# Optimization experiments

Measured on AMD Instinct MI355X. Metric: run time of the kernel, lower is better.

## Reference

```python
import jax, jax.numpy as jnp
import numpy as np

N = 8192      # nodes
K_NN = 32     # kNN neighbors (module default k=32)
E = N * 16    # edges for TAGConv graph
EPS = 1e-5    # BatchNorm eps


def setup_inputs() -> dict:
    key = jax.random.key(0)
    ks = iter(jax.random.split(key, 64))
    def lin(i, o):
        return jax.random.normal(next(ks), (i, o), jnp.float32) / np.float32(np.sqrt(i))
    def vec(c, scale=0.02):
        return jax.random.normal(next(ks), (c,), jnp.float32) * scale
    inp = {}
    inp["pos"] = jax.random.normal(next(ks), (N, 3), jnp.float32)
    inp["x"] = jax.random.normal(next(ks), (N, 4), jnp.float32)
    inp["edge_index"] = jax.random.randint(next(ks), (2, E), 0, N, jnp.int32)
    # conv1 edge-MLP [2*3, 64, 64, 64]
    inp["mlp1_W1"] = lin(6, 64)
    inp["mlp1_W23"] = jnp.stack([lin(64, 64), lin(64, 64)])
    inp["mlp1_b"] = jnp.stack([vec(64) for _ in range(3)])
    inp["mlp1_g"] = 1.0 + jnp.stack([vec(64) for _ in range(3)])
    inp["mlp1_beta"] = jnp.stack([vec(64) for _ in range(3)])
    # conv2 edge-MLP [2*64, 128]
    inp["mlp2_W"] = lin(128, 128); inp["mlp2_b"] = vec(128)
    inp["mlp2_g"] = 1.0 + vec(128); inp["mlp2_beta"] = vec(128)
    # lin1 MLP [128+64, 512]
    inp["lin1_W"] = lin(192, 512); inp["lin1_b"] = vec(512)
    inp["lin1_g"] = 1.0 + vec(512); inp["lin1_beta"] = vec(512)
    # TAGConv(4,64,K=3) and TAGConv(64,128,K=3): K+1 hop weights each, shared bias
    inp["tag1_W"] = jnp.stack([lin(4, 64) for _ in range(4)]); inp["tag1_b"] = vec(64)
    inp["tag2_W"] = jnp.stack([lin(64, 128) for _ in range(4)]); inp["tag2_b"] = vec(128)
    # lin_gcnn1 MLP [128+64, 512]
    inp["lin2_W"] = lin(192, 512); inp["lin2_b"] = vec(512)
    inp["lin2_g"] = 1.0 + vec(512); inp["lin2_beta"] = vec(512)
    # mix_output: MLP[1024,512] -> Dropout -> MLP[512,256] -> Dropout -> Lin(256,1)
    inp["mix1_W"] = lin(1024, 512); inp["mix1_b"] = vec(512)
    inp["mix1_g"] = 1.0 + vec(512); inp["mix1_beta"] = vec(512)
    inp["mix2_W"] = lin(512, 256); inp["mix2_b"] = vec(256)
    inp["mix2_g"] = 1.0 + vec(256); inp["mix2_beta"] = vec(256)
    inp["out_W"] = lin(256, 1); inp["out_b"] = vec(1)
    return inp


def _bn_relu_lin(h, W, b, g, beta):
    # Seq(Linear, ReLU, BatchNorm1d) with training-mode (batch) statistics
    h = jax.nn.relu(h @ W + b)
    mu = jnp.mean(h, axis=0)
    var = jnp.var(h, axis=0)
    return g * (h - mu) * jax.lax.rsqrt(var + EPS) + beta


def _knn_idx(x, k):
    # brute-force kNN (loop=False: self excluded); indices are non-differentiable
    x = jax.lax.stop_gradient(x)
    sq = jnp.sum(x * x, axis=1)
    d = sq[:, None] + sq[None, :] - 2.0 * (x @ x.T)   # [N,N] squared dists
    n = x.shape[0]
    d = d.at[jnp.arange(n), jnp.arange(n)].set(jnp.inf)
    _, idx = jax.lax.top_k(-d, k)
    return idx                                        # [N,k]


def _edge_conv(x, k, mlp_fn):
    # DynamicEdgeConv: kNN graph on x, message MLP([x_i, x_j - x_i]), max-aggregate
    idx = _knn_idx(x, k)
    xj = x[idx]                                       # [N,k,C]
    xi = jnp.broadcast_to(x[:, None, :], xj.shape)
    e = jnp.concatenate([xi, xj - xi], axis=-1).reshape(-1, 2 * x.shape[1])
    h = mlp_fn(e)                                     # [N*k, C_out]
    return jnp.max(h.reshape(x.shape[0], k, -1), axis=1)


def _tag_conv(x, W, b, row, col, norm):
    # TAGConv: out = sum_{m=0..K} (D^-1/2 A D^-1/2)^m x @ W_m + b
    out = x @ W[0]
    h = x
    for m in range(1, W.shape[0]):
        h = jax.ops.segment_sum(norm[:, None] * h[row], col, num_segments=x.shape[0])
        out = out + h @ W[m]
    return out + b


def reference(pos, x, edge_index, mlp1_W1, mlp1_W23, mlp1_b, mlp1_g, mlp1_beta,
              mlp2_W, mlp2_b, mlp2_g, mlp2_beta, lin1_W, lin1_b, lin1_g, lin1_beta,
              tag1_W, tag1_b, tag2_W, tag2_b, lin2_W, lin2_b, lin2_g, lin2_beta,
              mix1_W, mix1_b, mix1_g, mix1_beta, mix2_W, mix2_b, mix2_g, mix2_beta,
              out_W, out_b):
    def mlp1(e):
        h = _bn_relu_lin(e, mlp1_W1, mlp1_b[0], mlp1_g[0], mlp1_beta[0])
        h = _bn_relu_lin(h, mlp1_W23[0], mlp1_b[1], mlp1_g[1], mlp1_beta[1])
        return _bn_relu_lin(h, mlp1_W23[1], mlp1_b[2], mlp1_g[2], mlp1_beta[2])
    def mlp2(e):
        return _bn_relu_lin(e, mlp2_W, mlp2_b, mlp2_g, mlp2_beta)

    # --- DGCNN branch on positions ---
    x1 = _edge_conv(pos, K_NN, mlp1)                  # [N,64]
    x2 = _edge_conv(x1, K_NN, mlp2)                   # [N,128]
    out_dg = _bn_relu_lin(jnp.concatenate([x1, x2], axis=1),
                          lin1_W, lin1_b, lin1_g, lin1_beta)  # [N,512]

    # --- TAGConv branch on node features ---
    row, col = edge_index[0], edge_index[1]
    deg = jax.ops.segment_sum(jnp.ones(row.shape[0], x.dtype), col, num_segments=x.shape[0])
    dinv = jnp.where(deg > 0, jax.lax.rsqrt(jnp.maximum(deg, 1.0)), 0.0)
    norm = dinv[row] * dinv[col]
    g1 = jax.nn.relu(_tag_conv(x, tag1_W, tag1_b, row, col, norm))    # [N,64]
    g2 = jax.nn.relu(_tag_conv(g1, tag2_W, tag2_b, row, col, norm))   # [N,128]
    out_g = _bn_relu_lin(jnp.concatenate([g1, g2], axis=1),
                         lin2_W, lin2_b, lin2_g, lin2_beta)           # [N,512]

    # --- mix head (dropout = identity in eval) ---
    h = jnp.concatenate([out_dg, out_g], axis=1)      # [N,1024]
    h = _bn_relu_lin(h, mix1_W, mix1_b, mix1_g, mix1_beta)
    h = _bn_relu_lin(h, mix2_W, mix2_b, mix2_g, mix2_beta)
    return h @ out_W + out_b                          # [N,1]
```

## Files before the change

### kernel.cpp

```cpp
#include <hip/hip_runtime.h>
#include <cstdint>
#include <cstddef>

#define BN_EPS 1e-5f
#define K1CAP 1024
#define K2CAP 640

typedef short short8 __attribute__((ext_vector_type(8)));
typedef float f32x4 __attribute__((ext_vector_type(4)));
typedef unsigned long long ull;

__device__ __forceinline__ unsigned int ordf(float d) {
  unsigned int u = __float_as_uint(d);
  return (u >> 31) ? ~u : (u | 0x80000000u);
}
__device__ __forceinline__ unsigned short f2bf(float f) {
  unsigned u = __float_as_uint(f);
  u += 0x7fffu + ((u >> 16) & 1u);
  return (unsigned short)(u >> 16);
}
__device__ __forceinline__ float bf2f(unsigned short h) {
  return __uint_as_float(((unsigned)h) << 16);
}

#define BPAD 72

__global__ __launch_bounds__(256)
void mk_gemm_mfma(const float* __restrict__ A,
                  const short* __restrict__ A8h, const short* __restrict__ A8l,
                  const float* __restrict__ src, const int* __restrict__ gidx, int srcC,
                  const float* __restrict__ bnA,
                  const short* __restrict__ Wh, const short* __restrict__ Wl,
                  int ldk, int koff, int lda,
                  const float* __restrict__ bias,
                  float* __restrict__ C, short* __restrict__ Ch, short* __restrict__ Cl,
                  int ldc,
                  int M, int N, int K, int flags,
                  float* __restrict__ statsP,
                  float* __restrict__ mxp, float* __restrict__ mnp) {
  __shared__ short Ah[64][BPAD], Al[64][BPAD], Bh[64][BPAD], Bl[64][BPAD];
  __shared__ float ssum[64], ssq[64];
  int tid = threadIdx.x, lane = tid & 63, wid = tid >> 6;
  int wr = wid >> 1, wc = wid & 1;
  int r0 = blockIdx.x * 64, n0 = blockIdx.y * 64;
  int sr = tid >> 2, sc = (tid & 3) * 16;
  f32x4 zero4 = {0.f, 0.f, 0.f, 0.f};
  f32x4 acc[2][2] = {{zero4, zero4}, {zero4, zero4}};
  short8 rAh[2], rAl[2], rBh[2], rBl[2];

  auto stage = [&](int kt) {
    const short* bh = &Wh[(size_t)(n0 + sr) * ldk + koff + kt + sc];
    const short* bl = &Wl[(size_t)(n0 + sr) * ldk + koff + kt + sc];
    rBh[0] = *(const short8*)bh; rBh[1] = *(const short8*)(bh + 8);
    rBl[0] = *(const short8*)bl; rBl[1] = *(const short8*)(bl + 8);
    if (A8h) {
      const short* ah = &A8h[(size_t)(r0 + sr) * lda + kt + sc];
      const short* al = &A8l[(size_t)(r0 + sr) * lda + kt + sc];
      rAh[0] = *(const short8*)ah; rAh[1] = *(const short8*)(ah + 8);
      rAl[0] = *(const short8*)al; rAl[1] = *(const short8*)(al + 8);
    } else {
      float v[16];
      if (flags & 32) {
        int gr = r0 + sr;
        int i = gr >> 5; int j = gidx[gr];
        const float* pi = &A[(size_t)i * srcC + kt + sc];
        const float* pj = &src[(size_t)j * srcC + kt + sc];
        float va[16], vb[16];
        *(float4*)&va[0]  = *(const float4*)&pi[0];
        *(float4*)&va[4]  = *(const float4*)&pi[4];
        *(float4*)&va[8]  = *(const float4*)&pi[8];
        *(float4*)&va[12] = *(const float4*)&pi[12];
        *(float4*)&vb[0]  = *(const float4*)&pj[0];
        *(float4*)&vb[4]  = *(const float4*)&pj[4];
        *(float4*)&vb[8]  = *(const float4*)&pj[8];
        *(float4*)&vb[12] = *(const float4*)&pj[12];
#pragma unroll
        for (int e = 0; e < 16; ++e) v[e] = fmaxf(va[e] + vb[e], 0.f);
      } else {
        const float* ap = &A[(size_t)(r0 + sr) * lda + kt + sc];
        *(float4*)&v[0]  = *(const float4*)&ap[0];
        *(float4*)&v[4]  = *(const float4*)&ap[4];
        *(float4*)&v[8]  = *(const float4*)&ap[8];
        *(float4*)&v[12] = *(const float4*)&ap[12];
      }
      if (bnA) {
#pragma unroll
        for (int e = 0; e < 16; ++e) {
          int gk = kt + sc + e;
          v[e] = fmaf(bnA[gk], v[e], bnA[1024 + gk]);
        }
      }
#pragma unroll
      for (int e = 0; e < 16; ++e) {
        unsigned short h = f2bf(v[e]);
        rAh[e >> 3][e & 7] = (short)h;
        rAl[e >> 3][e & 7] = (short)f2bf(v[e] - bf2f(h));
      }
    }
  };

  stage(0);
  for (int kt = 0; kt < K; kt += 64) {
    *(short8*)&Ah[sr][sc]     = rAh[0];
    *(short8*)&Ah[sr][sc + 8] = rAh[1];
    *(short8*)&Al[sr][sc]     = rAl[0];
    *(short8*)&Al[sr][sc + 8] = rAl[1];
    *(short8*)&Bh[sr][sc]     = rBh[0];
    *(short8*)&Bh[sr][sc + 8] = rBh[1];
    *(short8*)&Bl[sr][sc]     = rBl[0];
    *(short8*)&Bl[sr][sc + 8] = rBl[1];
    __syncthreads();
    if (kt + 64 < K) stage(kt + 64);
    int ar = wr * 32 + (lane & 15);
    int br = wc * 32 + (lane & 15);
#pragma unroll
    for (int kk = 0; kk < 2; ++kk) {
      int kof = kk * 32 + (lane >> 4) * 8;
      short8 a_h[2], a_l[2], b_h[2], b_l[2];
#pragma unroll
      for (int t = 0; t < 2; ++t) {
        a_h[t] = *(const short8*)&Ah[ar + t * 16][kof];
        a_l[t] = *(const short8*)&Al[ar + t * 16][kof];
        b_h[t] = *(const short8*)&Bh[br + t * 16][kof];
        b_l[t] = *(const short8*)&Bl[br + t * 16][kof];
      }
#pragma unroll
      for (int mt = 0; mt < 2; ++mt)
#pragma unroll
        for (int nt = 0; nt < 2; ++nt) {
          acc[mt][nt] = __builtin_amdgcn_mfma_f32_16x16x32_bf16(a_h[mt], b_h[nt], acc[mt][nt], 0, 0, 0);
          acc[mt][nt] = __builtin_amdgcn_mfma_f32_16x16x32_bf16(a_h[mt], b_l[nt], acc[mt][nt], 0, 0, 0);
          acc[mt][nt] = __builtin_amdgcn_mfma_f32_16x16x32_bf16(a_l[mt], b_h[nt], acc[mt][nt], 0, 0, 0);
        }
    }
    __syncthreads();
  }
  bool dostat = (flags & 8) != 0, domx = (flags & 16) != 0;
  float lsum[2] = {0.f, 0.f}, lsq[2] = {0.f, 0.f};
  float lmx[2] = {-3.4e38f, -3.4e38f}, lmn[2] = {3.4e38f, 3.4e38f};
#pragma unroll
  for (int nt = 0; nt < 2; ++nt) {
    int gc = n0 + wc * 32 + nt * 16 + (lane & 15);
#pragma unroll
    for (int mt = 0; mt < 2; ++mt)
#pragma unroll
      for (int i = 0; i < 4; ++i) {
        int gr = r0 + wr * 32 + mt * 16 + (lane >> 4) * 4 + i;
        float v = acc[mt][nt][i];
        if (bias) v += bias[gc];
        if (flags & 1) v += C[(size_t)gr * ldc + gc];
        if (flags & 2) v = fmaxf(v, 0.f);
        if (!domx) {
          if (flags & 128) {
            int gj = srcC + gc;
            unsigned kk2 = (gr == gj) ? 0xFFFFFFFFu
                                      : ordf(src[gr] + src[gj] - 2.f * v);
            ((unsigned*)C)[(size_t)gr * ldc + gc] = kk2;
          } else if (flags & 64) {
            unsigned short hh = f2bf(v);
            Ch[(size_t)gr * ldc + gc] = (short)hh;
            Cl[(size_t)gr * ldc + gc] = (short)f2bf(v - bf2f(hh));
          } else {
            C[(size_t)gr * ldc + gc] = v;
          }
        }
        lsum[nt] += v; lsq[nt] = fmaf(v, v, lsq[nt]);
        lmx[nt] = fmaxf(lmx[nt], v); lmn[nt] = fminf(lmn[nt], v);
      }
  }
  if (dostat || domx) {
#pragma unroll
    for (int nt = 0; nt < 2; ++nt) {
#pragma unroll
      for (int m = 16; m <= 32; m <<= 1) {
        lsum[nt] += __shfl_xor(lsum[nt], m, 64);
        lsq[nt] += __shfl_xor(lsq[nt], m, 64);
        lmx[nt] = fmaxf(lmx[nt], __shfl_xor(lmx[nt], m, 64));
        lmn[nt] = fminf(lmn[nt], __shfl_xor(lmn[nt], m, 64));
      }
    }
    if (domx && lane < 16) {
      int node = blockIdx.x * 2 + wr;
#pragma unroll
      for (int nt = 0; nt < 2; ++nt) {
        int gc = n0 + wc * 32 + nt * 16 + lane;
        mxp[(size_t)node * N + gc] = lmx[nt];
        mnp[(size_t)node * N + gc] = lmn[nt];
      }
    }
    if (dostat) {
      if (tid < 64) { ssum[tid] = 0.f; ssq[tid] = 0.f; }
      __syncthreads();
      if (lane < 16) {
#pragma unroll
        for (int nt = 0; nt < 2; ++nt) {
          int ct = wc * 32 + nt * 16 + lane;
          atomicAdd(&ssum[ct], lsum[nt]);
          atomicAdd(&ssq[ct], lsq[nt]);
        }
      }
      __syncthreads();
      if (tid < 64) {
        int slot = blockIdx.x & 63;
        int gc = n0 + tid;
        atomicAdd(&statsP[(size_t)slot * 1024 + gc], ssum[tid]);
        atomicAdd(&statsP[(size_t)slot * 1024 + 512 + gc], ssq[tid]);
      }
    }
  }
}

__global__ void mk_wcvt(const float* __restrict__ W, short* __restrict__ Wh,
                        short* __restrict__ Wl, int K, int N) {
  int g = blockIdx.x * 256 + threadIdx.x;
  if (g >= K * N) return;
  int k = g / N, n = g - k * N;
  float v = W[g];
  unsigned short h = f2bf(v);
  Wh[(size_t)n * K + k] = (short)h;
  Wl[(size_t)n * K + k] = (short)f2bf(v - bf2f(h));
}
__global__ void mk_wcvts(const float* __restrict__ W, const float* __restrict__ a,
                         short* __restrict__ Wh, short* __restrict__ Wl, int K, int N) {
  int g = blockIdx.x * 256 + threadIdx.x;
  if (g >= K * N) return;
  int k = g / N, n = g - k * N;
  float v = a[k] * W[g];
  unsigned short h = f2bf(v);
  Wh[(size_t)n * K + k] = (short)h;
  Wl[(size_t)n * K + k] = (short)f2bf(v - bf2f(h));
}
__global__ void mk_biasfold(const float* __restrict__ W, const float* __restrict__ bv,
                            const float* __restrict__ b0, float* __restrict__ bo,
                            int K, int N) {
  int col = blockIdx.x * 4 + (threadIdx.x >> 6);
  int lane = threadIdx.x & 63;
  if (col >= N) return;
  float s = 0.f;
  for (int k = lane; k < K; k += 64) s = fmaf(bv[k], W[(size_t)k * N + col], s);
#pragma unroll
  for (int off = 32; off; off >>= 1) s += __shfl_xor(s, off, 64);
  if (lane == 0) bo[col] = b0[col] + s;
}
__global__ void mk_wcvt2(const float* __restrict__ W, short* __restrict__ Dh,
                         short* __restrict__ Dl, short* __restrict__ Vh,
                         short* __restrict__ Vl) {
  int g = blockIdx.x * 256 + threadIdx.x;
  if (g >= 64 * 128) return;
  int k = g >> 7, n = g & 127;
  float u = W[k * 128 + n], vv = W[(64 + k) * 128 + n];
  float d = u - vv;
  unsigned short h = f2bf(d);
  Dh[n * 64 + k] = (short)h; Dl[n * 64 + k] = (short)f2bf(d - bf2f(h));
  h = f2bf(vv);
  Vh[n * 64 + k] = (short)h; Vl[n * 64 + k] = (short)f2bf(vv - bf2f(h));
}

__global__ void mk_conv1nodes(const float* __restrict__ pos, const float* __restrict__ W1,
                              const float* __restrict__ b1, float* __restrict__ Pp,
                              float* __restrict__ Qn) {
  int g = blockIdx.x * 256 + threadIdx.x;
  if (g >= 8192 * 64) return;
  int i = g >> 6, c = g & 63;
  float p0 = pos[i * 3], p1 = pos[i * 3 + 1], p2 = pos[i * 3 + 2];
  float q = p0 * W1[192 + c] + p1 * W1[256 + c] + p2 * W1[320 + c];
  Qn[g] = q;
  Pp[g] = p0 * W1[c] + p1 * W1[64 + c] + p2 * W1[128 + c] - q + b1[c];
}

__global__ __launch_bounds__(256)
void mk_stats1(const float* __restrict__ Pp, const float* __restrict__ Qn,
               const int* __restrict__ idx1, float* __restrict__ statsP) {
  __shared__ int sidx[512];
  int tid = threadIdx.x;
  int c = tid & 63, grp = tid >> 6;
  int nb = blockIdx.x * 16;
  if (tid < 256) {
    sidx[tid] = idx1[nb * 32 + tid];
    sidx[tid + 256] = idx1[nb * 32 + 256 + tid];
  }
  __syncthreads();
  float s = 0.f, q = 0.f;
  for (int ln = 0; ln < 16; ++ln) {
    float pv = Pp[(size_t)(nb + ln) * 64 + c];
    for (int e = grp; e < 32; e += 4) {
      int j = sidx[ln * 32 + e];
      float v = fmaxf(pv + Qn[(size_t)j * 64 + c], 0.f);
      s += v; q = fmaf(v, v, q);
    }
  }
  int slot = (blockIdx.x * 4 + grp) & 63;
  atomicAdd(&statsP[(size_t)slot * 1024 + c], s);
  atomicAdd(&statsP[(size_t)slot * 1024 + 512 + c], q);
}

__global__ __launch_bounds__(128)
void mk_econv2(const float* __restrict__ R, const float* __restrict__ T,
               const int* __restrict__ st_i, float* __restrict__ mxp,
               float* __restrict__ mnp, float* __restrict__ statsP) {
  __shared__ int sidx[256];
  int tid = threadIdx.x;
  int nb = blockIdx.x * 8;
  sidx[tid] = st_i[nb * 32 + tid];
  sidx[tid + 128] = st_i[nb * 32 + 128 + tid];
  __syncthreads();
  float s = 0.f, q = 0.f;
  for (int ln = 0; ln < 8; ++ln) {
    int i = nb + ln;
    float rv = R[(size_t)i * 128 + tid];
    float mx = -3.4e38f, mn = 3.4e38f;
    for (int e = 0; e < 32; ++e) {
      int j = sidx[ln * 32 + e];
      float v = fmaxf(rv + T[(size_t)j * 128 + tid], 0.f);
      mx = fmaxf(mx, v); mn = fminf(mn, v);
      s += v; q = fmaf(v, v, q);
    }
    mxp[(size_t)i * 128 + tid] = mx;
    mnp[(size_t)i * 128 + tid] = mn;
  }
  int slot = blockIdx.x & 63;
  atomicAdd(&statsP[(size_t)slot * 1024 + tid], s);
  atomicAdd(&statsP[(size_t)slot * 1024 + 512 + tid], q);
}

__global__ void mk_bnfinS(const float* __restrict__ sb, const float* __restrict__ g,
                          const float* __restrict__ beta, float* __restrict__ bno,
                          float Minv, int Cdim) {
  int c = blockIdx.x * 256 + threadIdx.x;
  if (c >= Cdim) return;
  float s = 0.f, q = 0.f;
  for (int sl = 0; sl < 64; ++sl) {
    s += sb[(size_t)sl * 1024 + c];
    q += sb[(size_t)sl * 1024 + 512 + c];
  }
  float mu = s * Minv;
  float var = q * Minv - mu * mu;
  float a = g[c] * rsqrtf(var + BN_EPS);
  bno[c] = a;
  bno[1024 + c] = beta[c] - a * mu;
}

__global__ void mk_finx1(const float* __restrict__ mx, const float* __restrict__ mn,
                         const float* __restrict__ bn, float* __restrict__ xc,
                         short* __restrict__ x1h, short* __restrict__ x1l) {
  int g = blockIdx.x * 256 + threadIdx.x;
  if (g >= 8192 * 64) return;
  int i = g >> 6, c = g & 63;
  float a = bn[c], b = bn[1024 + c];
  float v = (a > 0.f) ? fmaf(a, mx[g], b) : fmaf(a, mn[g], b);
  xc[(size_t)i * 192 + c] = v;
  unsigned short h = f2bf(v);
  x1h[g] = (short)h;
  x1l[g] = (short)f2bf(v - bf2f(h));
}
__global__ void mk_finx2(const float* __restrict__ mx, const float* __restrict__ mn,
                         const float* __restrict__ bn, float* __restrict__ xcB) {
  int g = blockIdx.x * 256 + threadIdx.x;
  if (g >= 8192 * 128) return;
  int i = g >> 7, c = g & 127;
  float a = bn[c], b = bn[1024 + c];
  xcB[(size_t)i * 192 + c] = (a > 0.f) ? fmaf(a, mx[g], b) : fmaf(a, mn[g], b);
}

__global__ void mk_posq(const float* __restrict__ pos, float4* __restrict__ posq) {
  int i = blockIdx.x * 256 + threadIdx.x;
  if (i >= 8192) return;
  float x = pos[i * 3], y = pos[i * 3 + 1], z = pos[i * 3 + 2];
  float s = fmaf(z, z, fmaf(y, y, x * x));
  posq[i] = make_float4(x, y, z, s);
}

__device__ __forceinline__ unsigned wave_kth8(unsigned v) {
  unsigned T = 0;
#pragma unroll
  for (int b = 31; b >= 0; --b) {
    unsigned cand = T | (1u << b);
    int c = __popcll(__ballot(v < cand));
    if (c < 8) T = cand;
  }
  return T;
}

__global__ __launch_bounds__(256)
void mk_knn1(const float4* __restrict__ posq, int* __restrict__ idxout) {
  __shared__ ull buf[K1CAP];
  __shared__ unsigned Tw[4];
  __shared__ unsigned cnt;
  int q = blockIdx.x, tid = threadIdx.x;
  int lane = tid & 63, wid = tid >> 6;
  float4 pq = posq[q];
  if (tid == 0) cnt = 0;
  unsigned key[32];
  unsigned vmin = 0xFFFFFFFFu;
#pragma unroll
  for (int c = 0; c < 32; ++c) {
    int j = c * 256 + tid;
    float4 pj = posq[j];
    float d = pq.w + pj.w - 2.f * (pq.x * pj.x + pq.y * pj.y + pq.z * pj.z);
    unsigned k = (j == q) ? 0xFFFFFFFFu : ordf(d);
    key[c] = k;
    vmin = vmin < k ? vmin : k;
  }
  unsigned T = wave_kth8(vmin);
  if (lane == 0) Tw[wid] = T;
  __syncthreads();
  unsigned Tmax = max(max(Tw[0], Tw[1]), max(Tw[2], Tw[3]));
#pragma unroll
  for (int c = 0; c < 32; ++c) {
    if (key[c] <= Tmax) {
      int j = c * 256 + tid;
      unsigned s = atomicAdd(&cnt, 1u);
      if (s < K1CAP) buf[s] = (((ull)key[c]) << 32) | (unsigned)j;
    }
  }
  __syncthreads();
  int m = cnt < (unsigned)K1CAP ? (int)cnt : K1CAP;
  for (int e = tid; e < m; e += 256) {
    ull mine = buf[e];
    int rank = 0;
    for (int f = 0; f < m; ++f) rank += (buf[f] < mine) ? 1 : 0;
    if (rank < 32) idxout[q * 32 + rank] = (int)(unsigned)(mine & 0xFFFFFFFFu);
  }
}

__global__ __launch_bounds__(256)
void mk_knn2(const unsigned* __restrict__ Kb, int c0, int first,
             unsigned* __restrict__ st_k, int* __restrict__ st_i) {
  __shared__ ull buf[K2CAP];
  __shared__ unsigned Tw[4];
  __shared__ unsigned cnt;
  int q = blockIdx.x, tid = threadIdx.x;
  int lane = tid & 63, wid = tid >> 6;
  if (tid == 0) cnt = 0;
  unsigned key[16];
  unsigned vmin = 0xFFFFFFFFu;
#pragma unroll
  for (int c = 0; c < 16; ++c) {
    unsigned k = Kb[(size_t)q * 4096 + c * 256 + tid];
    key[c] = k;
    vmin = vmin < k ? vmin : k;
  }
  unsigned T = wave_kth8(vmin);
  if (lane == 0) Tw[wid] = T;
  __syncthreads();
  unsigned Tmax = max(max(Tw[0], Tw[1]), max(Tw[2], Tw[3]));
#pragma unroll
  for (int c = 0; c < 16; ++c) {
    if (key[c] <= Tmax) {
      int j = c0 + c * 256 + tid;
      unsigned s = atomicAdd(&cnt, 1u);
      if (s < K2CAP) buf[s] = (((ull)key[c]) << 32) | (unsigned)j;
    }
  }
  if (!first && tid < 32) {
    ull k = (((ull)st_k[q * 32 + tid]) << 32) | (unsigned)st_i[q * 32 + tid];
    unsigned s = atomicAdd(&cnt, 1u);
    if (s < K2CAP) buf[s] = k;
  }
  __syncthreads();
  int m = cnt < (unsigned)K2CAP ? (int)cnt : K2CAP;
  for (int e = tid; e < m; e += 256) {
    ull mine = buf[e];
    int rank = 0;
    for (int f = 0; f < m; ++f) rank += (buf[f] < mine) ? 1 : 0;
    if (rank < 32) {
      st_k[q * 32 + rank] = (unsigned)(mine >> 32);
      st_i[q * 32 + rank] = (int)(unsigned)(mine & 0xFFFFFFFFu);
    }
  }
}

#define GBM 64
#define GBN 64
#define GBK 16

__global__ __launch_bounds__(256)
void mk_gemm(const float* __restrict__ A, const float* __restrict__ W, int ldw,
             const float* __restrict__ bias, float* __restrict__ C, int ldc,
             int M, int N, int K, int flags) {
  __shared__ float As[GBK][GBM + 4];
  __shared__ float Ws[GBK][GBN];
  int tid = threadIdx.x;
  int r0 = blockIdx.x * GBM, n0 = blockIdx.y * GBN;
  int ty = tid >> 4, tx = tid & 15;
  float acc[4][4] = {};
  for (int kt = 0; kt < K; kt += GBK) {
#pragma unroll
    for (int it = 0; it < 4; ++it) {
      int l = it * 256 + tid;
      int r = l >> 4, kk = l & 15;
      int gr = r0 + r, gk = kt + kk;
      float v = 0.f;
      if (gk < K && gr < M) v = A[(size_t)gr * K + gk];
      As[kk][r] = v;
      int kw = l >> 6, nw = l & 63;
      int gkw = kt + kw;
      Ws[kw][nw] = (gkw < K && (n0 + nw) < N) ? W[(size_t)gkw * ldw + n0 + nw] : 0.f;
    }
    __syncthreads();
#pragma unroll
    for (int kk = 0; kk < GBK; ++kk) {
      float4 a4 = *(const float4*)&As[kk][ty * 4];
      float4 b4 = *(const float4*)&Ws[kk][tx * 4];
      float av[4] = {a4.x, a4.y, a4.z, a4.w};
      float bv[4] = {b4.x, b4.y, b4.z, b4.w};
#pragma unroll
      for (int i = 0; i < 4; ++i)
#pragma unroll
        for (int j = 0; j < 4; ++j)
          acc[i][j] = fmaf(av[i], bv[j], acc[i][j]);
    }
    __syncthreads();
  }
#pragma unroll
  for (int i = 0; i < 4; ++i) {
    int gr = r0 + ty * 4 + i;
    if (gr >= M) continue;
#pragma unroll
    for (int j = 0; j < 4; ++j) {
      int gc = n0 + tx * 4 + j;
      if (gc >= N) continue;
      float v = acc[i][j];
      if (bias) v += bias[gc];
      if (flags & 1) v += C[(size_t)gr * ldc + gc];
      if (flags & 2) v = fmaxf(v, 0.f);
      C[(size_t)gr * ldc + gc] = v;
    }
  }
}

__global__ void mk_sqnorm(const float* __restrict__ x, int ld, float* __restrict__ sq,
                          int Npts, int Cdim) {
  int i = blockIdx.x * blockDim.x + threadIdx.x;
  if (i >= Npts) return;
  float s = 0.f;
  for (int c = 0; c < Cdim; ++c) { float v = x[(size_t)i * ld + c]; s = fmaf(v, v, s); }
  sq[i] = s;
}

__global__ void mk_count(const int* __restrict__ col, int* __restrict__ cnt, int E) {
  int e = blockIdx.x * 256 + threadIdx.x;
  if (e < E) atomicAdd(&cnt[col[e]], 1);
}
__global__ __launch_bounds__(1024)
void mk_scan(const int* __restrict__ cnt, int* __restrict__ offp,
             int* __restrict__ cur, float* __restrict__ dinvf) {
  __shared__ int wsum[16];
  __shared__ int wexc[16];
  int t = threadIdx.x, lane = t & 63, w = t >> 6;
  int v[8]; int s = 0;
  int base = t * 8;
#pragma unroll
  for (int k = 0; k < 8; ++k) { v[k] = s; s += cnt[base + k]; }
  int sc = s;
#pragma unroll
  for (int off2 = 1; off2 < 64; off2 <<= 1) {
    int n = __shfl_up(sc, off2, 64);
    if (lane >= off2) sc += n;
  }
  if (lane == 63) wsum[w] = sc;
  __syncthreads();
  if (w == 0) {
    int x = (lane < 16) ? wsum[lane] : 0;
    int scx = x;
#pragma unroll
    for (int off2 = 1; off2 < 16; off2 <<= 1) {
      int n = __shfl_up(scx, off2, 64);
      if (lane >= off2) scx += n;
    }
    if (lane < 16) wexc[lane] = scx - x;
  }
  __syncthreads();
  int texc = wexc[w] + (sc - s);
#pragma unroll
  for (int k = 0; k < 8; ++k) {
    int o = texc + v[k];
    offp[base + k] = o;
    cur[base + k] = o;
    int d = cnt[base + k];
    dinvf[base + k] = (d > 0) ? rsqrtf((float)(d < 1 ? 1 : d)) : 0.f;
  }
  if (t == 1023) offp[8192] = texc + s;
}
__global__ void mk_fill(const int* __restrict__ row, const int* __restrict__ col,
                        const float* __restrict__ dinvf, int* __restrict__ cur,
                        int* __restrict__ crow, float* __restrict__ cw, int E) {
  int e = blockIdx.x * 256 + threadIdx.x;
  if (e >= E) return;
  int c = col[e], r = row[e];
  int s = atomicAdd(&cur[c], 1);
  crow[s] = r;
  cw[s] = dinvf[r] * dinvf[c];
}
__global__ void mk_prop64(const float* __restrict__ in, int in_ld,
                          const int* __restrict__ offp, const int* __restrict__ crow,
                          const float* __restrict__ cw, float* __restrict__ out, int out_ld) {
  int gid = blockIdx.x * 256 + threadIdx.x;
  if (gid >= 8192 * 16) return;
  int col = gid >> 4, c4 = (gid & 15) * 4;
  int s0 = offp[col], s1 = offp[col + 1];
  float a0 = 0, a1 = 0, a2 = 0, a3 = 0;
  for (int s = s0; s < s1; ++s) {
    int r = crow[s]; float w = cw[s];
    float4 v = *(const float4*)&in[(size_t)r * in_ld + c4];
    a0 = fmaf(w, v.x, a0); a1 = fmaf(w, v.y, a1);
    a2 = fmaf(w, v.z, a2); a3 = fmaf(w, v.w, a3);
  }
  float4 o = {a0, a1, a2, a3};
  *(float4*)&out[(size_t)col * out_ld + c4] = o;
}
__global__ void mk_prop4(const float* __restrict__ in, int in_ld,
                         const int* __restrict__ offp, const int* __restrict__ crow,
                         const float* __restrict__ cw, float* __restrict__ out, int out_ld) {
  int col = blockIdx.x * 256 + threadIdx.x;
  if (col >= 8192) return;
  int s0 = offp[col], s1 = offp[col + 1];
  float a0 = 0, a1 = 0, a2 = 0, a3 = 0;
  for (int s = s0; s < s1; ++s) {
    int r = crow[s]; float w = cw[s];
    float4 v = *(const float4*)&in[(size_t)r * in_ld];
    a0 = fmaf(w, v.x, a0); a1 = fmaf(w, v.y, a1);
    a2 = fmaf(w, v.z, a2); a3 = fmaf(w, v.w, a3);
  }
  float4 o = {a0, a1, a2, a3};
  *(float4*)&out[(size_t)col * out_ld] = o;
}
__global__ void mk_pack4(const float* __restrict__ xin, float* __restrict__ H1) {
  int g = blockIdx.x * 256 + threadIdx.x;
  if (g >= 8192 * 4) return;
  H1[(size_t)(g >> 2) * 16 + (g & 3)] = xin[g];
}
__global__ void mk_copy64(const float* __restrict__ gcv, float* __restrict__ H2) {
  int g = blockIdx.x * 256 + threadIdx.x;
  if (g >= 8192 * 64) return;
  H2[(size_t)(g >> 6) * 256 + (g & 63)] = gcv[(size_t)(g >> 6) * 192 + (g & 63)];
}

__global__ __launch_bounds__(256)
void mk_gemv_out(const float* __restrict__ h, const float* __restrict__ bn,
                 const float* __restrict__ w, const float* __restrict__ b,
                 float* __restrict__ out, int Npts) {
  int row = blockIdx.x * 4 + (threadIdx.x >> 6);
  int lane = threadIdx.x & 63;
  if (row >= Npts) return;
  int c = lane * 4;
  float4 v = *(const float4*)&h[(size_t)row * 256 + c];
  float s = (bn[c] * v.x + bn[1024 + c]) * w[c]
          + (bn[c + 1] * v.y + bn[1024 + c + 1]) * w[c + 1]
          + (bn[c + 2] * v.z + bn[1024 + c + 2]) * w[c + 2]
          + (bn[c + 3] * v.w + bn[1024 + c + 3]) * w[c + 3];
#pragma unroll
  for (int off = 32; off; off >>= 1) s += __shfl_xor(s, off, 64);
  if (lane == 0) out[row] = s + b[0];
}

extern "C" void kernel_launch(void* const* d_in, const int* in_sizes, int n_in,
                              void* d_out, int out_size, void* d_ws, size_t ws_size,
                              hipStream_t stream) {
  const int N = 8192;
  const int NE = N * 32;
  const float* pos = (const float*)d_in[0];
  const float* xin = (const float*)d_in[1];
  const int* ei = (const int*)d_in[2];
  const int E = in_sizes[2] / 2;
  const int* erow = ei;
  const int* ecol = ei + E;
  const float* mlp1_W1  = (const float*)d_in[3];
  const float* mlp1_W23 = (const float*)d_in[4];
  const float* mlp1_b   = (const float*)d_in[5];
  const float* mlp1_g   = (const float*)d_in[6];
  const float* mlp1_be  = (const float*)d_in[7];
  const float* mlp2_W   = (const float*)d_in[8];
  const float* mlp2_b   = (const float*)d_in[9];
  const float* mlp2_g   = (const float*)d_in[10];
  const float* mlp2_be  = (const float*)d_in[11];
  const float* lin1_W   = (const float*)d_in[12];
  const float* lin1_b   = (const float*)d_in[13];
  const float* lin1_g   = (const float*)d_in[14];
  const float* lin1_be  = (const float*)d_in[15];
  const float* tag1_W   = (const float*)d_in[16];
  const float* tag1_b   = (const float*)d_in[17];
  const float* tag2_W   = (const float*)d_in[18];
  const float* tag2_b   = (const float*)d_in[19];
  const float* lin2_W   = (const float*)d_in[20];
  const float* lin2_b   = (const float*)d_in[21];
  const float* lin2_g   = (const float*)d_in[22];
  const float* lin2_be  = (const float*)d_in[23];
  const float* mix1_W   = (const float*)d_in[24];
  const float* mix1_b   = (const float*)d_in[25];
  const float* mix1_g   = (const float*)d_in[26];
  const float* mix1_be  = (const float*)d_in[27];
  const float* mix2_W   = (const float*)d_in[28];
  const float* mix2_b   = (const float*)d_in[29];
  const float* mix2_g   = (const float*)d_in[30];
  const float* mix2_be  = (const float*)d_in[31];
  const float* outW     = (const float*)d_in[32];
  const float* outB     = (const float*)d_in[33];

  char* base = (char*)d_ws;
  size_t off = 0;
  auto alloc = [&](size_t b) -> void* {
    void* p = base + off;
    off += (b + 255) & ~(size_t)255;
    return p;
  };
  float* BIG = (float*)alloc(134217728ull);
  short* h2_h  = (short*)BIG;
  short* h2_l  = (short*)((char*)BIG + 33554432);
  unsigned* Kb = (unsigned*)BIG;
  short* mhcat_h = (short*)BIG;
  short* mhcat_l = (short*)((char*)BIG + 16777216);
  short* mh1_h   = (short*)((char*)BIG + 33554432);
  short* mh1_l   = (short*)((char*)BIG + 41943040);
  float* mh2     = (float*)((char*)BIG + 50331648);
  float* H2      = BIG + 16777216;
  int*   idx1 = (int*)alloc((size_t)NE * 4);
  unsigned* st_k = (unsigned*)alloc((size_t)NE * 4);
  int*   st_i = (int*)alloc((size_t)NE * 4);
  float* xc  = (float*)alloc((size_t)N * 192 * 4);
  float* gc  = (float*)alloc((size_t)N * 192 * 4);
  float4* posq = (float4*)alloc((size_t)N * 16);
  float* sqx = (float*)alloc((size_t)N * 4);
  float* Pp  = (float*)alloc((size_t)N * 64 * 4);
  float* Qn  = (float*)alloc((size_t)N * 64 * 4);
  float* Rb  = (float*)alloc((size_t)N * 128 * 4);
  float* Tb  = (float*)alloc((size_t)N * 128 * 4);
  float* mx1 = (float*)alloc((size_t)N * 64 * 4);
  float* mn1 = (float*)alloc((size_t)N * 64 * 4);
  float* mx2 = (float*)alloc((size_t)N * 128 * 4);
  float* mn2 = (float*)alloc((size_t)N * 128 * 4);
  float* H1  = (float*)alloc((size_t)N * 16 * 4);
  float* dinvf = (float*)alloc((size_t)N * 4);
  int* cnt     = (int*)alloc((size_t)N * 4);
  int* csr_off = (int*)alloc((size_t)(N + 1) * 4);
  int* cursor  = (int*)alloc((size_t)N * 4);
  int* csr_row = (int*)alloc((size_t)E * 4);
  float* csr_w = (float*)alloc((size_t)E * 4);
  float* slotAll = (float*)alloc((size_t)8 * 64 * 1024 * 4);
  auto slot = [&](int i) { return slotAll + (size_t)i * 64 * 1024; };
  float* bnb = (float*)alloc(8 * 2048 * 4);
  auto bnp = [&](int i) { return bnb + (size_t)i * 2048; };
  float* bnM = bnp(4);
  float* bias1f = (float*)alloc(512 * 4);
  float* bias2f = (float*)alloc(256 * 4);
  float* biasA  = (float*)alloc(64 * 4);
  float* biasB  = (float*)alloc(64 * 4);
  auto salloc = [&](size_t n) { return (short*)alloc(n * 2); };
  short* w23a_h = salloc(4096);   short* w23a_l = salloc(4096);
  short* w23b_h = salloc(4096);   short* w23b_l = salloc(4096);
  short* wd2_h  = salloc(8192);   short* wd2_l  = salloc(8192);
  short* wv2_h  = salloc(8192);   short* wv2_l  = salloc(8192);
  short* wl1_h  = salloc(98304);  short* wl1_l  = salloc(98304);
  short* wt2_h  = salloc(32768);  short* wt2_l  = salloc(32768);
  short* wl2_h  = salloc(98304);  short* wl2_l  = salloc(98304);
  short* wx1_h  = salloc(524288); short* wx1_l  = salloc(524288);
  short* wx2_h  = salloc(131072); short* wx2_l  = salloc(131072);
  short* x1h    = salloc(524288); short* x1l    = salloc(524288);

  auto gemmF = [&](const float* A, const short* A8h, const short* A8l,
                   const float* src, const int* gidx, int srcC, const float* bnA,
                   const short* Wh_, const short* Wl_, int ldk, int koff, int lda,
                   const float* bias, float* Cp, short* Chp, short* Clp, int ldc,
                   int M, int Nn, int Kk, int flags,
                   float* stP = nullptr, float* mxP = nullptr, float* mnP = nullptr) {
    dim3 g(M / 64, Nn / 64);
    mk_gemm_mfma<<<g, 256, 0, stream>>>(A, A8h, A8l, src, gidx, srcC, bnA,
                                        Wh_, Wl_, ldk, koff, lda, bias, Cp, Chp, Clp, ldc,
                                        M, Nn, Kk, flags, stP, mxP, mnP);
  };
  auto wcvt = [&](const float* W, short* Wh_, short* Wl_, int Kk, int Nn) {
    mk_wcvt<<<(Kk * Nn + 255) / 256, 256, 0, stream>>>(W, Wh_, Wl_, Kk, Nn);
  };

  hipMemsetAsync(slotAll, 0, (size_t)8 * 64 * 1024 * 4, stream);
  hipMemsetAsync(cnt, 0, (size_t)N * 4, stream);
  mk_wcvt2<<<(64 * 128 + 255) / 256, 256, 0, stream>>>(mlp2_W, wd2_h, wd2_l, wv2_h, wv2_l);
  wcvt(lin1_W, wl1_h, wl1_l, 192, 512);
  wcvt(tag2_W, wt2_h, wt2_l, 256, 128);
  wcvt(lin2_W, wl2_h, wl2_l, 192, 512);

  mk_posq<<<32, 256, 0, stream>>>(pos, posq);
  mk_knn1<<<N, 256, 0, stream>>>(posq, idx1);

  mk_conv1nodes<<<(N * 64 + 255) / 256, 256, 0, stream>>>(pos, mlp1_W1, mlp1_b, Pp, Qn);
  mk_stats1<<<512, 256, 0, stream>>>(Pp, Qn, idx1, slot(0));
  mk_bnfinS<<<1, 256, 0, stream>>>(slot(0), mlp1_g, mlp1_be, bnp(0), 1.f / NE, 64);
  mk_wcvts<<<(64 * 64 + 255) / 256, 256, 0, stream>>>(mlp1_W23, bnp(0), w23a_h, w23a_l, 64, 64);
  mk_biasfold<<<16, 256, 0, stream>>>(mlp1_W23, bnp(0) + 1024, mlp1_b + 64, biasA, 64, 64);
  gemmF(Pp, nullptr, nullptr, Qn, idx1, 64, nullptr,
        w23a_h, w23a_l, 64, 0, 64, biasA, nullptr, h2_h, h2_l, 64,
        NE, 64, 64, 2 | 8 | 32 | 64, slot(1));
  mk_bnfinS<<<1, 256, 0, stream>>>(slot(1), mlp1_g + 64, mlp1_be + 64, bnp(1), 1.f / NE, 64);
  mk_wcvts<<<(64 * 64 + 255) / 256, 256, 0, stream>>>(mlp1_W23 + 4096, bnp(1), w23b_h, w23b_l, 64, 64);
  mk_biasfold<<<16, 256, 0, stream>>>(mlp1_W23 + 4096, bnp(1) + 1024, mlp1_b + 128, biasB, 64, 64);
  gemmF(nullptr, h2_h, h2_l, nullptr, nullptr, 0, nullptr,
        w23b_h, w23b_l, 64, 0, 64, biasB, nullptr, nullptr, nullptr, 64,
        NE, 64, 64, 2 | 8 | 16, slot(2), mx1, mn1);
  mk_bnfinS<<<1, 256, 0, stream>>>(slot(2), mlp1_g + 128, mlp1_be + 128, bnp(2), 1.f / NE, 64);
  mk_finx1<<<(N * 64 + 255) / 256, 256, 0, stream>>>(mx1, mn1, bnp(2), xc, x1h, x1l);

  mk_sqnorm<<<32, 256, 0, stream>>>(xc, 192, sqx, N, 64);
  for (int c = 0; c < 2; ++c) {
    gemmF(nullptr, x1h, x1l, sqx, nullptr, c * 4096, nullptr,
          x1h + (size_t)c * 4096 * 64, x1l + (size_t)c * 4096 * 64, 64, 0, 64,
          nullptr, (float*)Kb, nullptr, nullptr, 4096, N, 4096, 64, 128);
    mk_knn2<<<N, 256, 0, stream>>>(Kb, c * 4096, c == 0 ? 1 : 0, st_k, st_i);
  }

  gemmF(nullptr, x1h, x1l, nullptr, nullptr, 0, nullptr,
        wd2_h, wd2_l, 64, 0, 64, mlp2_b, Rb, nullptr, nullptr, 128, N, 128, 64, 0);
  gemmF(nullptr, x1h, x1l, nullptr, nullptr, 0, nullptr,
        wv2_h, wv2_l, 64, 0, 64, nullptr, Tb, nullptr, nullptr, 128, N, 128, 64, 0);
  mk_econv2<<<N / 8, 128, 0, stream>>>(Rb, Tb, st_i, mx2, mn2, slot(3));
  mk_bnfinS<<<1, 256, 0, stream>>>(slot(3), mlp2_g, mlp2_be, bnp(3), 1.f / NE, 128);
  mk_finx2<<<(N * 128 + 255) / 256, 256, 0, stream>>>(mx2, mn2, bnp(3), xc + 64);

  gemmF(xc, nullptr, nullptr, nullptr, nullptr, 0, nullptr,
        wl1_h, wl1_l, 192, 0, 192, lin1_b, nullptr, mhcat_h, mhcat_l, 1024,
        N, 512, 192, 2 | 8 | 64, slot(4));
  mk_bnfinS<<<2, 256, 0, stream>>>(slot(4), lin1_g, lin1_be, bnM, 1.f / N, 512);

  mk_count<<<(E + 255) / 256, 256, 0, stream>>>(ecol, cnt, E);
  mk_scan<<<1, 1024, 0, stream>>>(cnt, csr_off, cursor, dinvf);
  mk_fill<<<(E + 255) / 256, 256, 0, stream>>>(erow, ecol, dinvf, cursor, csr_row, csr_w, E);
  mk_pack4<<<(N * 4 + 255) / 256, 256, 0, stream>>>(xin, H1);
  mk_prop4<<<32, 256, 0, stream>>>(xin, 4, csr_off, csr_row, csr_w, H1 + 4, 16);
  mk_prop4<<<32, 256, 0, stream>>>(H1 + 4, 16, csr_off, csr_row, csr_w, H1 + 8, 16);
  mk_prop4<<<32, 256, 0, stream>>>(H1 + 8, 16, csr_off, csr_row, csr_w, H1 + 12, 16);
  mk_gemm<<<dim3(128, 1), 256, 0, stream>>>(H1, tag1_W, 64, tag1_b, gc, 192, N, 64, 16, 2);
  mk_copy64<<<(N * 64 + 255) / 256, 256, 0, stream>>>(gc, H2);
  mk_prop64<<<512, 256, 0, stream>>>(gc, 192, csr_off, csr_row, csr_w, H2 + 64, 256);
  mk_prop64<<<512, 256, 0, stream>>>(H2 + 64, 256, csr_off, csr_row, csr_w, H2 + 128, 256);
  mk_prop64<<<512, 256, 0, stream>>>(H2 + 128, 256, csr_off, csr_row, csr_w, H2 + 192, 256);
  gemmF(H2, nullptr, nullptr, nullptr, nullptr, 0, nullptr,
        wt2_h, wt2_l, 256, 0, 256, tag2_b, gc + 64, nullptr, nullptr, 192,
        N, 128, 256, 2);
  gemmF(gc, nullptr, nullptr, nullptr, nullptr, 0, nullptr,
        wl2_h, wl2_l, 192, 0, 192, lin2_b, nullptr, mhcat_h + 512, mhcat_l + 512, 1024,
        N, 512, 192, 2 | 8 | 64, slot(5));
  mk_bnfinS<<<2, 256, 0, stream>>>(slot(5), lin2_g, lin2_be, bnM + 512, 1.f / N, 512);

  mk_wcvts<<<(1024 * 512 + 255) / 256, 256, 0, stream>>>(mix1_W, bnM, wx1_h, wx1_l, 1024, 512);
  mk_biasfold<<<128, 256, 0, stream>>>(mix1_W, bnM + 1024, mix1_b, bias1f, 1024, 512);
  gemmF(nullptr, mhcat_h, mhcat_l, nullptr, nullptr, 0, nullptr,
        wx1_h, wx1_l, 1024, 0, 1024, bias1f, nullptr, mh1_h, mh1_l, 512,
        N, 512, 1024, 2 | 8 | 64, slot(6));
  mk_bnfinS<<<2, 256, 0, stream>>>(slot(6), mix1_g, mix1_be, bnp(6), 1.f / N, 512);
  mk_wcvts<<<(512 * 256 + 255) / 256, 256, 0, stream>>>(mix2_W, bnp(6), wx2_h, wx2_l, 512, 256);
  mk_biasfold<<<64, 256, 0, stream>>>(mix2_W, bnp(6) + 1024, mix2_b, bias2f, 512, 256);
  gemmF(nullptr, mh1_h, mh1_l, nullptr, nullptr, 0, nullptr,
        wx2_h, wx2_l, 512, 0, 512, bias2f, mh2, nullptr, nullptr, 256,
        N, 256, 512, 2 | 8, slot(7));
  mk_bnfinS<<<1, 256, 0, stream>>>(slot(7), mix2_g, mix2_be, bnp(7), 1.f / N, 256);
  mk_gemv_out<<<N / 4, 256, 0, stream>>>(mh2, bnp(7), outW, outB, (float*)d_out, N);
}
```

Before: 686.4 us.

## Replace dense kNN distance matrix with two-pass threshold-filtered candidate selection

The second kNN used to write full 4096-wide distance-key blocks to global memory and then scan them per query. It now runs the distance GEMM twice. The first pass writes only per-block column minima, from which a per-row threshold (the 32nd smallest of the 128 block minima) is derived. The second pass recomputes the distances and appends only keys at or below that threshold into per-row candidate buffers, which a rank kernel then sorts. This removes the large key-matrix write and read, at the cost of a duplicated GEMM, global atomics, and a capped candidate buffer that could overflow.

```diff
diff --git a/kernel.cpp b/kernel.cpp
--- a/kernel.cpp
+++ b/kernel.cpp
@@ -4,7 +4,7 @@
 
 #define BN_EPS 1e-5f
 #define K1CAP 1024
-#define K2CAP 640
+#define KPCAP 512
 
 typedef short short8 __attribute__((ext_vector_type(8)));
 typedef float f32x4 __attribute__((ext_vector_type(4)));
@@ -135,6 +135,60 @@
     }
     __syncthreads();
   }
+
+  if (flags & 128) {
+    unsigned* tm = (unsigned*)ssum;
+    if (tid < 64) tm[tid] = 0xFFFFFFFFu;
+    __syncthreads();
+#pragma unroll
+    for (int mt = 0; mt < 2; ++mt)
+#pragma unroll
+      for (int i = 0; i < 4; ++i) {
+        int lr = wr * 32 + mt * 16 + (lane >> 4) * 4 + i;
+        int gr = r0 + lr;
+        unsigned kmin = 0xFFFFFFFFu;
+#pragma unroll
+        for (int nt = 0; nt < 2; ++nt) {
+          int gc = n0 + wc * 32 + nt * 16 + (lane & 15);
+          float v = acc[mt][nt][i];
+          unsigned kk2 = (gr == gc) ? 0xFFFFFFFFu : ordf(src[gr] + src[gc] - 2.f * v);
+          kmin = kmin < kk2 ? kmin : kk2;
+        }
+#pragma unroll
+        for (int off = 1; off < 16; off <<= 1) {
+          unsigned o = (unsigned)__shfl_xor((int)kmin, off, 64);
+          kmin = kmin < o ? kmin : o;
+        }
+        if ((lane & 15) == 0) atomicMin(&tm[lr], kmin);
+      }
+    __syncthreads();
+    if (tid < 64)
+      ((unsigned*)C)[(size_t)(r0 + tid) * ldc + blockIdx.y] = tm[tid];
+    return;
+  }
+  if (flags & 256) {
+    const unsigned* Trow = (const unsigned*)gidx;
+    unsigned* cntp = (unsigned*)mxp;
+    ull* bufp = (ull*)mnp;
+#pragma unroll
+    for (int mt = 0; mt < 2; ++mt)
+#pragma unroll
+      for (int nt = 0; nt < 2; ++nt)
+#pragma unroll
+        for (int i = 0; i < 4; ++i) {
+          int gr = r0 + wr * 32 + mt * 16 + (lane >> 4) * 4 + i;
+          int gc = n0 + wc * 32 + nt * 16 + (lane & 15);
+          float v = acc[mt][nt][i];
+          unsigned kk2 = (gr == gc) ? 0xFFFFFFFFu : ordf(src[gr] + src[gc] - 2.f * v);
+          if (kk2 <= Trow[gr]) {
+            unsigned s = atomicAdd(&cntp[gr], 1u);
+            if (s < (unsigned)KPCAP)
+              bufp[(size_t)gr * KPCAP + s] = (((ull)kk2) << 32) | (unsigned)gc;
+          }
+        }
+    return;
+  }
+
   bool dostat = (flags & 8) != 0, domx = (flags & 16) != 0;
   float lsum[2] = {0.f, 0.f}, lsq[2] = {0.f, 0.f};
   float lmx[2] = {-3.4e38f, -3.4e38f}, lmn[2] = {3.4e38f, 3.4e38f};
@@ -151,12 +205,7 @@
         if (flags & 1) v += C[(size_t)gr * ldc + gc];
         if (flags & 2) v = fmaxf(v, 0.f);
         if (!domx) {
-          if (flags & 128) {
-            int gj = srcC + gc;
-            unsigned kk2 = (gr == gj) ? 0xFFFFFFFFu
-                                      : ordf(src[gr] + src[gj] - 2.f * v);
-            ((unsigned*)C)[(size_t)gr * ldc + gc] = kk2;
-          } else if (flags & 64) {
+          if (flags & 64) {
             unsigned short hh = f2bf(v);
             Ch[(size_t)gr * ldc + gc] = (short)hh;
             Cl[(size_t)gr * ldc + gc] = (short)f2bf(v - bf2f(hh));
@@ -424,49 +473,34 @@
 }
 
 __global__ __launch_bounds__(256)
-void mk_knn2(const unsigned* __restrict__ Kb, int c0, int first,
-             unsigned* __restrict__ st_k, int* __restrict__ st_i) {
-  __shared__ ull buf[K2CAP];
-  __shared__ unsigned Tw[4];
-  __shared__ unsigned cnt;
-  int q = blockIdx.x, tid = threadIdx.x;
-  int lane = tid & 63, wid = tid >> 6;
-  if (tid == 0) cnt = 0;
-  unsigned key[16];
-  unsigned vmin = 0xFFFFFFFFu;
-#pragma unroll
-  for (int c = 0; c < 16; ++c) {
-    unsigned k = Kb[(size_t)q * 4096 + c * 256 + tid];
-    key[c] = k;
-    vmin = vmin < k ? vmin : k;
-  }
-  unsigned T = wave_kth8(vmin);
-  if (lane == 0) Tw[wid] = T;
-  __syncthreads();
-  unsigned Tmax = max(max(Tw[0], Tw[1]), max(Tw[2], Tw[3]));
-#pragma unroll
-  for (int c = 0; c < 16; ++c) {
-    if (key[c] <= Tmax) {
-      int j = c0 + c * 256 + tid;
-      unsigned s = atomicAdd(&cnt, 1u);
-      if (s < K2CAP) buf[s] = (((ull)key[c]) << 32) | (unsigned)j;
-    }
-  }
-  if (!first && tid < 32) {
-    ull k = (((ull)st_k[q * 32 + tid]) << 32) | (unsigned)st_i[q * 32 + tid];
-    unsigned s = atomicAdd(&cnt, 1u);
-    if (s < K2CAP) buf[s] = k;
-  }
-  __syncthreads();
-  int m = cnt < (unsigned)K2CAP ? (int)cnt : K2CAP;
-  for (int e = tid; e < m; e += 256) {
-    ull mine = buf[e];
+void mk_thresh(const unsigned* __restrict__ Tmin, unsigned* __restrict__ Trow,
+               unsigned* __restrict__ cnt) {
+  int tid = threadIdx.x, lane = tid & 63, wid = tid >> 6;
+  int row = blockIdx.x * 4 + wid;
+  unsigned t0 = Tmin[(size_t)row * 128 + lane];
+  unsigned t1 = Tmin[(size_t)row * 128 + 64 + lane];
+  unsigned T = 0;
+#pragma unroll
+  for (int b = 31; b >= 0; --b) {
+    unsigned cand = T | (1u << b);
+    int c = __popcll(__ballot(t0 < cand)) + __popcll(__ballot(t1 < cand));
+    if (c < 32) T = cand;
+  }
+  if (lane == 0) { Trow[row] = T; cnt[row] = 0u; }
+}
+
+__global__ __launch_bounds__(256)
+void mk_rank(const unsigned* __restrict__ cnt, const ull* __restrict__ buf,
+             int* __restrict__ idxout) {
+  int tid = threadIdx.x, lane = tid & 63, wid = tid >> 6;
+  int row = blockIdx.x * 4 + wid;
+  unsigned cm = cnt[row];
+  int m = cm < (unsigned)KPCAP ? (int)cm : KPCAP;
+  for (int e = lane; e < m; e += 64) {
+    ull mine = buf[(size_t)row * KPCAP + e];
     int rank = 0;
-    for (int f = 0; f < m; ++f) rank += (buf[f] < mine) ? 1 : 0;
-    if (rank < 32) {
-      st_k[q * 32 + rank] = (unsigned)(mine >> 32);
-      st_i[q * 32 + rank] = (int)(unsigned)(mine & 0xFFFFFFFFu);
-    }
+    for (int f = 0; f < m; ++f) rank += (buf[(size_t)row * KPCAP + f] < mine) ? 1 : 0;
+    if (rank < 32) idxout[row * 32 + rank] = (int)(unsigned)(mine & 0xFFFFFFFFu);
   }
 }
 
@@ -707,7 +741,8 @@
   float* BIG = (float*)alloc(134217728ull);
   short* h2_h  = (short*)BIG;
   short* h2_l  = (short*)((char*)BIG + 33554432);
-  unsigned* Kb = (unsigned*)BIG;
+  ull*   kbuf  = (ull*)BIG;
+  unsigned* Tmin = (unsigned*)((char*)BIG + 33554432);
   short* mhcat_h = (short*)BIG;
   short* mhcat_l = (short*)((char*)BIG + 16777216);
   short* mh1_h   = (short*)((char*)BIG + 33554432);
@@ -715,8 +750,9 @@
   float* mh2     = (float*)((char*)BIG + 50331648);
   float* H2      = BIG + 16777216;
   int*   idx1 = (int*)alloc((size_t)NE * 4);
-  unsigned* st_k = (unsigned*)alloc((size_t)NE * 4);
   int*   st_i = (int*)alloc((size_t)NE * 4);
+  unsigned* Trow = (unsigned*)alloc((size_t)N * 4);
+  unsigned* kcnt = (unsigned*)alloc((size_t)N * 4);
   float* xc  = (float*)alloc((size_t)N * 192 * 4);
   float* gc  = (float*)alloc((size_t)N * 192 * 4);
   float4* posq = (float4*)alloc((size_t)N * 16);
@@ -800,12 +836,15 @@
   mk_finx1<<<(N * 64 + 255) / 256, 256, 0, stream>>>(mx1, mn1, bnp(2), xc, x1h, x1l);
 
   mk_sqnorm<<<32, 256, 0, stream>>>(xc, 192, sqx, N, 64);
-  for (int c = 0; c < 2; ++c) {
-    gemmF(nullptr, x1h, x1l, sqx, nullptr, c * 4096, nullptr,
-          x1h + (size_t)c * 4096 * 64, x1l + (size_t)c * 4096 * 64, 64, 0, 64,
-          nullptr, (float*)Kb, nullptr, nullptr, 4096, N, 4096, 64, 128);
-    mk_knn2<<<N, 256, 0, stream>>>(Kb, c * 4096, c == 0 ? 1 : 0, st_k, st_i);
-  }
+  gemmF(nullptr, x1h, x1l, sqx, nullptr, 0, nullptr,
+        x1h, x1l, 64, 0, 64,
+        nullptr, (float*)Tmin, nullptr, nullptr, 128, N, N, 64, 128);
+  mk_thresh<<<N / 4, 256, 0, stream>>>(Tmin, Trow, kcnt);
+  gemmF(nullptr, x1h, x1l, sqx, (const int*)Trow, 0, nullptr,
+        x1h, x1l, 64, 0, 64,
+        nullptr, nullptr, nullptr, nullptr, 0, N, N, 64, 256,
+        nullptr, (float*)kcnt, (float*)kbuf);
+  mk_rank<<<N / 4, 256, 0, stream>>>(kcnt, kbuf, st_i);
 
   gemmF(nullptr, x1h, x1l, nullptr, nullptr, 0, nullptr,
         wd2_h, wd2_l, 64, 0, 64, mlp2_b, Rb, nullptr, nullptr, 128, N, 128, 64, 0);
```

After: 791.7 us. 1.15x slower.
